# Optimization experiments

Measured on AMD Instinct MI355X. Metric: run time of the kernel, lower is better.

The kernel has to match this reference:

```python
import jax, jax.numpy as jnp
import numpy as np

N_NODES = 50000
N_EDGES = 600000
IN_CH = 128
HID = 128
OUT_CH = 1
N_GRAPHS = 64


def setup_inputs() -> dict:
    key = jax.random.key(0)
    ks = jax.random.split(key, 16)
    inp = {
        "x": jax.random.normal(ks[0], (N_NODES, IN_CH), dtype=jnp.float32),
        "edge_index": jax.random.randint(ks[1], (2, N_EDGES), 0, N_NODES, dtype=jnp.int64),
        "edge_weight": jax.random.uniform(ks[2], (N_EDGES,), dtype=jnp.float32),
        "batch": jnp.sort(jax.random.randint(ks[3], (N_NODES,), 0, N_GRAPHS, dtype=jnp.int64)),
    }
    # SAGEConv params: lin_l (neighbor-aggregate path, has bias) and lin_r (root path)
    dims = [(IN_CH, HID), (HID, HID), (HID, HID), (HID, HID)]
    for i, (din, dout) in enumerate(dims, start=1):
        s = 1.0 / np.sqrt(din)
        inp[f"Wl{i}"] = jax.random.uniform(ks[3 + 2 * i], (din, dout), minval=-s, maxval=s, dtype=jnp.float32)
        inp[f"Wr{i}"] = jax.random.uniform(ks[4 + 2 * i], (din, dout), minval=-s, maxval=s, dtype=jnp.float32)
        inp[f"b{i}"] = jnp.zeros((dout,), dtype=jnp.float32)
    s = 1.0 / np.sqrt(HID)
    inp["Wc"] = jax.random.uniform(ks[14], (HID, OUT_CH), minval=-s, maxval=s, dtype=jnp.float32)
    inp["bc"] = jnp.zeros((OUT_CH,), dtype=jnp.float32)
    return inp


def _sage_conv(x, src, dst, Wl, Wr, b):
    # mean aggregation of source-node features at each destination node
    msg = x[src]  # [E, d] gather
    agg = jax.ops.segment_sum(msg, dst, num_segments=N_NODES)
    cnt = jax.ops.segment_sum(jnp.ones((src.shape[0],), x.dtype), dst, num_segments=N_NODES)
    agg = agg / jnp.maximum(cnt, 1.0)[:, None]
    return agg @ Wl + b + x @ Wr


def reference(x, edge_index, edge_weight, batch,
              Wl1, Wr1, b1, Wl2, Wr2, b2, Wl3, Wr3, b3, Wl4, Wr4, b4, Wc, bc):
    src, dst = edge_index[0], edge_index[1]
    h = jax.nn.relu(_sage_conv(x, src, dst, Wl1, Wr1, b1))
    h = jax.nn.relu(_sage_conv(h, src, dst, Wl2, Wr2, b2))
    h = jax.nn.relu(_sage_conv(h, src, dst, Wl3, Wr3, b3))
    h = jax.nn.relu(_sage_conv(h, src, dst, Wl4, Wr4, b4))
    # global mean pool over graphs
    pooled = jax.ops.segment_sum(h, batch, num_segments=N_GRAPHS)
    gcnt = jax.ops.segment_sum(jnp.ones((N_NODES,), h.dtype), batch, num_segments=N_GRAPHS)
    pooled = pooled / jnp.maximum(gcnt, 1.0)[:, None]  # [G, HID]
    return jax.nn.sigmoid(pooled @ Wc + bc)  # [G, 1]
```

## Files before the change

kernel.cpp:

```cpp
#include <hip/hip_runtime.h>
#include <math.h>

#define NND 50000
#define LNP 50048
#define NED 600000
#define CD  128
#define NG  64
#define NBLK 196
#define GROWS 64

typedef short s8v  __attribute__((ext_vector_type(8)));
typedef float f4v  __attribute__((ext_vector_type(4)));
typedef float f2v  __attribute__((ext_vector_type(2)));
typedef unsigned short u16x4 __attribute__((ext_vector_type(4)));
typedef unsigned short u16x8 __attribute__((ext_vector_type(8)));

static __device__ __forceinline__ unsigned short f2bf(float f) {
  union { float f; unsigned u; } v; v.f = f;
  unsigned r = v.u + 0x7fffu + ((v.u >> 16) & 1u);
  return (unsigned short)(r >> 16);
}
static __device__ __forceinline__ float bf2f(unsigned short h) {
  union { unsigned u; float f; } v; v.u = ((unsigned)h) << 16; return v.f;
}
static __device__ __forceinline__ unsigned f2fp8x4(float a, float b, float c, float d) {
  int r = __builtin_amdgcn_cvt_pk_fp8_f32(a, b, 0, false);
  r = __builtin_amdgcn_cvt_pk_fp8_f32(c, d, r, true);
  return (unsigned)r;
}
static __device__ __forceinline__ void g2lds(const unsigned short* g, unsigned short* l) {
  __builtin_amdgcn_global_load_lds(
      (const __attribute__((address_space(1))) unsigned*)g,
      (__attribute__((address_space(3))) unsigned*)l, 16, 0, 0);
}

__global__ void counti_k(const int* __restrict__ idx, int* __restrict__ cnt, int n) {
  int t = blockIdx.x * blockDim.x + threadIdx.x;
  if (t < n) atomicAdd(&cnt[idx[t]], 1);
}

__global__ __launch_bounds__(256) void bsum_k(const int* __restrict__ cnt,
                                              int* __restrict__ bsum) {
  __shared__ int s[256];
  int i = blockIdx.x * 256 + threadIdx.x;
  s[threadIdx.x] = (i < NND) ? cnt[i] : 0;
  __syncthreads();
  for (int off = 128; off > 0; off >>= 1) {
    if (threadIdx.x < off) s[threadIdx.x] += s[threadIdx.x + off];
    __syncthreads();
  }
  if (threadIdx.x == 0) bsum[blockIdx.x] = s[0];
}

__global__ __launch_bounds__(256) void bscan_k(const int* __restrict__ bsum,
                                               int* __restrict__ boff,
                                               int* __restrict__ offs,
                                               const int* __restrict__ batch,
                                               int* __restrict__ gb) {
  __shared__ int s[256];
  int t = threadIdx.x;
  if (t <= NG) {
    int lo = 0, hi = NND;
    while (lo < hi) {
      int mid = (lo + hi) >> 1;
      if (batch[mid] < t) lo = mid + 1; else hi = mid;
    }
    gb[t] = lo;
  }
  s[t] = (t < NBLK) ? bsum[t] : 0;
  __syncthreads();
  for (int off = 1; off < 256; off <<= 1) {
    int v = (t >= off) ? s[t - off] : 0;
    __syncthreads();
    s[t] += v;
    __syncthreads();
  }
  if (t < NBLK) boff[t] = (t == 0) ? 0 : s[t - 1];
  if (t == NBLK - 1) offs[NND] = s[t];
}

__global__ __launch_bounds__(256) void escan_k(const int* __restrict__ cnt,
                                               const int* __restrict__ boff,
                                               int* __restrict__ offs,
                                               int* __restrict__ cur) {
  __shared__ int s[256];
  int i = blockIdx.x * 256 + threadIdx.x;
  int t = threadIdx.x;
  int v = (i < NND) ? cnt[i] : 0;
  s[t] = v;
  __syncthreads();
  for (int off = 1; off < 256; off <<= 1) {
    int u = (t >= off) ? s[t - off] : 0;
    __syncthreads();
    s[t] += u;
    __syncthreads();
  }
  if (i < NND) {
    int excl = s[t] - v + boff[blockIdx.x];
    offs[i] = excl;
    cur[i]  = excl;
  }
}

__global__ void fill_k(const int* __restrict__ src, const int* __restrict__ dst,
                       int* __restrict__ cur, int* __restrict__ csr) {
  int e = blockIdx.x * blockDim.x + threadIdx.x;
  if (e >= NED) return;
  int d = dst[e];
  int pos = atomicAdd(&cur[d], 1);
  csr[pos] = src[e];
}

struct WPtrs { const float* w[8]; unsigned short* wt[8]; };
__global__ void prep_k(const float* __restrict__ x, unsigned short* __restrict__ xb,
                       unsigned* __restrict__ x8, WPtrs p) {
  int t = blockIdx.x * blockDim.x + threadIdx.x;
  if (t < NND * 32) {
    float4 v = reinterpret_cast<const float4*>(x)[t];
    u16x4 o;
    o.x = f2bf(v.x); o.y = f2bf(v.y); o.z = f2bf(v.z); o.w = f2bf(v.w);
    reinterpret_cast<u16x4*>(xb)[t] = o;
    x8[t] = f2fp8x4(v.x, v.y, v.z, v.w);
  } else {
    int u = t - NND * 32;
    if (u < 8 * CD * CD) {
      int m = u >> 14, r = u & (CD * CD - 1);
      int n = r >> 7, k = r & 127;
      p.wt[m][r] = f2bf(p.w[m][k * CD + n]);
    }
  }
}

__global__ __launch_bounds__(256) void agg_k(const unsigned* __restrict__ xq,
                                             const int* __restrict__ csr,
                                             const int* __restrict__ offs,
                                             unsigned short* __restrict__ ab) {
  const int team = (blockIdx.x * 256 + threadIdx.x) >> 4;
  const int tl   = threadIdx.x & 15;
  const int e0 = offs[team], e1 = offs[team + 1];
  const unsigned* base = xq + tl * 2;
  f2v a01 = {0.f, 0.f}, a23 = {0.f, 0.f}, a45 = {0.f, 0.f}, a67 = {0.f, 0.f};
  int e = e0;
  for (; e + 8 <= e1; e += 8) {
    int s[8];
#pragma unroll
    for (int j = 0; j < 8; ++j) s[j] = csr[e + j];
    uint2 v[8];
#pragma unroll
    for (int j = 0; j < 8; ++j)
      v[j] = *reinterpret_cast<const uint2*>(base + (size_t)s[j] * 32);
#pragma unroll
    for (int j = 0; j < 8; ++j) {
      a01 += __builtin_amdgcn_cvt_pk_f32_fp8(v[j].x, false);
      a23 += __builtin_amdgcn_cvt_pk_f32_fp8(v[j].x, true);
      a45 += __builtin_amdgcn_cvt_pk_f32_fp8(v[j].y, false);
      a67 += __builtin_amdgcn_cvt_pk_f32_fp8(v[j].y, true);
    }
  }
  for (; e + 4 <= e1; e += 4) {
    int s[4];
#pragma unroll
    for (int j = 0; j < 4; ++j) s[j] = csr[e + j];
    uint2 v[4];
#pragma unroll
    for (int j = 0; j < 4; ++j)
      v[j] = *reinterpret_cast<const uint2*>(base + (size_t)s[j] * 32);
#pragma unroll
    for (int j = 0; j < 4; ++j) {
      a01 += __builtin_amdgcn_cvt_pk_f32_fp8(v[j].x, false);
      a23 += __builtin_amdgcn_cvt_pk_f32_fp8(v[j].x, true);
      a45 += __builtin_amdgcn_cvt_pk_f32_fp8(v[j].y, false);
      a67 += __builtin_amdgcn_cvt_pk_f32_fp8(v[j].y, true);
    }
  }
  for (; e < e1; ++e) {
    uint2 v = *reinterpret_cast<const uint2*>(base + (size_t)csr[e] * 32);
    a01 += __builtin_amdgcn_cvt_pk_f32_fp8(v.x, false);
    a23 += __builtin_amdgcn_cvt_pk_f32_fp8(v.x, true);
    a45 += __builtin_amdgcn_cvt_pk_f32_fp8(v.y, false);
    a67 += __builtin_amdgcn_cvt_pk_f32_fp8(v.y, true);
  }
  const float invd = 1.0f / fmaxf((float)(e1 - e0), 1.0f);
  u16x8 o;
  o[0] = f2bf(a01.x * invd); o[1] = f2bf(a01.y * invd);
  o[2] = f2bf(a23.x * invd); o[3] = f2bf(a23.y * invd);
  o[4] = f2bf(a45.x * invd); o[5] = f2bf(a45.y * invd);
  o[6] = f2bf(a67.x * invd); o[7] = f2bf(a67.y * invd);
  *reinterpret_cast<u16x8*>(ab + (size_t)team * CD + tl * 8) = o;
}

__global__ __launch_bounds__(256) void gemm3_k(
    const unsigned short* __restrict__ ab, const unsigned short* __restrict__ xb,
    const unsigned short* __restrict__ WlT, const unsigned short* __restrict__ WrT,
    const float* __restrict__ bias, unsigned short* __restrict__ hb,
    unsigned char* __restrict__ h8) {
  __shared__ unsigned short abuf[GROWS * CD];
  __shared__ unsigned short xbuf[GROWS * CD];

  const int tid  = threadIdx.x;
  const int wave = tid >> 6;
  const int lane = tid & 63;
  const int quad = lane >> 4;
  const int l16  = lane & 15;
  const size_t rbase = (size_t)blockIdx.x * GROWS;

#pragma unroll
  for (int j = 0; j < 4; ++j) {
    const int s = j * 256 + tid;
    const size_t goff = (rbase + (s >> 4)) * CD + (s & 15) * 8;
    g2lds(ab + goff, &abuf[(size_t)s * 8]);
    g2lds(xb + goff, &xbuf[(size_t)s * 8]);
  }

  s8v bL[2][4], bR[2][4];
#pragma unroll
  for (int nt = 0; nt < 2; ++nt) {
    const int n = wave * 32 + nt * 16 + l16;
#pragma unroll
    for (int kk = 0; kk < 4; ++kk) {
      size_t woff = (size_t)n * CD + kk * 32 + quad * 8;
      bL[nt][kk] = *reinterpret_cast<const s8v*>(WlT + woff);
      bR[nt][kk] = *reinterpret_cast<const s8v*>(WrT + woff);
    }
  }
  const float bv0 = bias[wave * 32 + l16];
  const float bv1 = bias[wave * 32 + 16 + l16];

  __syncthreads();

#pragma unroll
  for (int rt = 0; rt < GROWS / 16; ++rt) {
    const unsigned short* arow = abuf + (rt * 16 + l16) * CD + quad * 8;
    const unsigned short* xrow = xbuf + (rt * 16 + l16) * CD + quad * 8;
    f4v acc0 = {}, acc1 = {};
#pragma unroll
    for (int kk = 0; kk < 4; ++kk) {
      s8v aA = *reinterpret_cast<const s8v*>(arow + kk * 32);
      s8v aX = *reinterpret_cast<const s8v*>(xrow + kk * 32);
      acc0 = __builtin_amdgcn_mfma_f32_16x16x32_bf16(aA, bL[0][kk], acc0, 0, 0, 0);
      acc0 = __builtin_amdgcn_mfma_f32_16x16x32_bf16(aX, bR[0][kk], acc0, 0, 0, 0);
      acc1 = __builtin_amdgcn_mfma_f32_16x16x32_bf16(aA, bL[1][kk], acc1, 0, 0, 0);
      acc1 = __builtin_amdgcn_mfma_f32_16x16x32_bf16(aX, bR[1][kk], acc1, 0, 0, 0);
    }
    const size_t row0 = rbase + rt * 16 + quad * 4;
    const int c0 = wave * 32 + l16;
#pragma unroll
    for (int r = 0; r < 4; ++r) {
      const size_t row = row0 + r;
      float v0 = fmaxf(acc0[r] + bv0, 0.0f);
      float v1 = fmaxf(acc1[r] + bv1, 0.0f);
      hb[row * CD + c0]      = f2bf(v0);
      hb[row * CD + c0 + 16] = f2bf(v1);
      if (h8) {
        int p0 = __builtin_amdgcn_cvt_pk_fp8_f32(v0, v0, 0, false);
        int p1 = __builtin_amdgcn_cvt_pk_fp8_f32(v1, v1, 0, false);
        h8[row * CD + c0]      = (unsigned char)p0;
        h8[row * CD + c0 + 16] = (unsigned char)p1;
      }
    }
  }
}

__global__ __launch_bounds__(128) void pool3_k(const unsigned short* __restrict__ h,
                                               const int* __restrict__ batch,
                                               float* __restrict__ pooled) {
  const int c  = threadIdx.x;
  const int r0 = blockIdx.x * 32;
  const int rend = (r0 + 32 < NND) ? r0 + 32 : NND;
  const int g0 = batch[r0];
  const int g1 = batch[rend - 1];
  if (g0 == g1) {
    float acc = 0.f;
#pragma unroll
    for (int i = 0; i < 32; ++i) {
      int row = r0 + i;
      if (row < rend) acc += bf2f(h[(size_t)row * CD + c]);
    }
    atomicAdd(&pooled[g0 * CD + c], acc);
  } else {
    float acc = 0.f;
    int gcur = g0;
    for (int row = r0; row < rend; ++row) {
      int g = batch[row];
      if (g != gcur) {
        atomicAdd(&pooled[gcur * CD + c], acc);
        acc = 0.f; gcur = g;
      }
      acc += bf2f(h[(size_t)row * CD + c]);
    }
    atomicAdd(&pooled[gcur * CD + c], acc);
  }
}

__global__ void final_k(const float* __restrict__ pooled, const int* __restrict__ gb,
                        const float* __restrict__ Wc, const float* __restrict__ bc,
                        float* __restrict__ out) {
  int g = blockIdx.x;
  int lane = threadIdx.x;
  float part = pooled[g * CD + lane] * Wc[lane] +
               pooled[g * CD + 64 + lane] * Wc[64 + lane];
#pragma unroll
  for (int off = 32; off > 0; off >>= 1) part += __shfl_down(part, off, 64);
  if (lane == 0) {
    float cnt = (float)(gb[g + 1] - gb[g]);
    float z = part / fmaxf(cnt, 1.0f) + bc[0];
    out[g] = 1.0f / (1.0f + expf(-z));
  }
}

extern "C" void kernel_launch(void* const* d_in, const int* in_sizes, int n_in,
                              void* d_out, int out_size, void* d_ws, size_t ws_size,
                              hipStream_t stream) {
  const float* x   = (const float*)d_in[0];
  const int*   ei  = (const int*)d_in[1];
  const int*   src = ei;
  const int*   dst = ei + NED;
  const int*   batch = (const int*)d_in[3];
  const float* Wc = (const float*)d_in[16];
  const float* bc = (const float*)d_in[17];
  float* out = (float*)d_out;

  char* w = (char*)d_ws;
  auto alloc = [&](size_t bytes) {
    char* p = w; w += (bytes + 255) & ~(size_t)255; return p;
  };
  int* cnti = (int*)alloc(NND * 4);
  float* pooled = (float*)alloc(NG * CD * 4);
  size_t zspan = (size_t)(w - (char*)cnti);
  int* offs = (int*)alloc((NND + 1) * 4);
  int* cur  = (int*)alloc(NND * 4);
  int* csr  = (int*)alloc((size_t)NED * 4);
  int* gb   = (int*)alloc((NG + 1) * 4);
  int* bsum = (int*)alloc(256 * 4);
  int* boff = (int*)alloc(256 * 4);
  unsigned short* xb0 = (unsigned short*)alloc((size_t)LNP * CD * 2);
  unsigned short* xb1 = (unsigned short*)alloc((size_t)LNP * CD * 2);
  unsigned short* ab  = (unsigned short*)alloc((size_t)LNP * CD * 2);
  unsigned char* x8a = (unsigned char*)alloc((size_t)LNP * CD);
  unsigned char* x8b = (unsigned char*)alloc((size_t)LNP * CD);
  WPtrs wp;
  for (int i = 0; i < 4; ++i) {
    wp.w[2 * i]     = (const float*)d_in[4 + 3 * i];
    wp.w[2 * i + 1] = (const float*)d_in[5 + 3 * i];
  }
  for (int i = 0; i < 8; ++i) wp.wt[i] = (unsigned short*)alloc(CD * CD * 2);
  const float* bs[4] = {(const float*)d_in[6],  (const float*)d_in[9],
                        (const float*)d_in[12], (const float*)d_in[15]};

  hipMemsetAsync(cnti, 0, zspan, stream);

  counti_k<<<(NED + 255) / 256, 256, 0, stream>>>(dst, cnti, NED);
  bsum_k<<<NBLK, 256, 0, stream>>>(cnti, bsum);
  bscan_k<<<1, 256, 0, stream>>>(bsum, boff, offs, batch, gb);
  escan_k<<<NBLK, 256, 0, stream>>>(cnti, boff, offs, cur);
  fill_k<<<(NED + 255) / 256, 256, 0, stream>>>(src, dst, cur, csr);

  prep_k<<<(NND * 32 + 8 * CD * CD + 255) / 256, 256, 0, stream>>>(
      x, xb0, (unsigned*)x8a, wp);

  unsigned short* xcur = xb0;
  unsigned short* xnxt = xb1;
  unsigned char* qcur = x8a;
  unsigned char* qnxt = x8b;
  const int ggrid = LNP / GROWS;
  for (int l = 0; l < 4; ++l) {
    agg_k<<<NND * 16 / 256, 256, 0, stream>>>((const unsigned*)qcur, csr, offs, ab);
    gemm3_k<<<ggrid, 256, 0, stream>>>(ab, xcur, wp.wt[2 * l], wp.wt[2 * l + 1],
                                       bs[l], xnxt, (l < 3) ? qnxt : nullptr);
    unsigned short* t = xcur; xcur = xnxt; xnxt = t;
    unsigned char* q = qcur; qcur = qnxt; qnxt = q;
  }

  pool3_k<<<(NND + 31) / 32, 128, 0, stream>>>(xcur, batch, pooled);
  final_k<<<NG, 64, 0, stream>>>(pooled, gb, Wc, bc, out);
}
```

Measured before the change: 327.2 us.

## Fuse neighbor aggregation into SAGE GEMM kernel and fold degree count into prep

```diff
diff --git a/kernel.cpp b/kernel.cpp
--- a/kernel.cpp
+++ b/kernel.cpp
@@ -32,11 +32,6 @@
   __builtin_amdgcn_global_load_lds(
       (const __attribute__((address_space(1))) unsigned*)g,
       (__attribute__((address_space(3))) unsigned*)l, 16, 0, 0);
-}
-
-__global__ void counti_k(const int* __restrict__ idx, int* __restrict__ cnt, int n) {
-  int t = blockIdx.x * blockDim.x + threadIdx.x;
-  if (t < n) atomicAdd(&cnt[idx[t]], 1);
 }
 
 __global__ __launch_bounds__(256) void bsum_k(const int* __restrict__ cnt,
@@ -113,7 +108,8 @@
 
 struct WPtrs { const float* w[8]; unsigned short* wt[8]; };
 __global__ void prep_k(const float* __restrict__ x, unsigned short* __restrict__ xb,
-                       unsigned* __restrict__ x8, WPtrs p) {
+                       unsigned* __restrict__ x8, WPtrs p,
+                       const int* __restrict__ dst, int* __restrict__ cnt) {
   int t = blockIdx.x * blockDim.x + threadIdx.x;
   if (t < NND * 32) {
     float4 v = reinterpret_cast<const float4*>(x)[t];
@@ -127,70 +123,16 @@
       int m = u >> 14, r = u & (CD * CD - 1);
       int n = r >> 7, k = r & 127;
       p.wt[m][r] = f2bf(p.w[m][k * CD + n]);
-    }
-  }
-}
-
-__global__ __launch_bounds__(256) void agg_k(const unsigned* __restrict__ xq,
-                                             const int* __restrict__ csr,
-                                             const int* __restrict__ offs,
-                                             unsigned short* __restrict__ ab) {
-  const int team = (blockIdx.x * 256 + threadIdx.x) >> 4;
-  const int tl   = threadIdx.x & 15;
-  const int e0 = offs[team], e1 = offs[team + 1];
-  const unsigned* base = xq + tl * 2;
-  f2v a01 = {0.f, 0.f}, a23 = {0.f, 0.f}, a45 = {0.f, 0.f}, a67 = {0.f, 0.f};
-  int e = e0;
-  for (; e + 8 <= e1; e += 8) {
-    int s[8];
-#pragma unroll
-    for (int j = 0; j < 8; ++j) s[j] = csr[e + j];
-    uint2 v[8];
-#pragma unroll
-    for (int j = 0; j < 8; ++j)
-      v[j] = *reinterpret_cast<const uint2*>(base + (size_t)s[j] * 32);
-#pragma unroll
-    for (int j = 0; j < 8; ++j) {
-      a01 += __builtin_amdgcn_cvt_pk_f32_fp8(v[j].x, false);
-      a23 += __builtin_amdgcn_cvt_pk_f32_fp8(v[j].x, true);
-      a45 += __builtin_amdgcn_cvt_pk_f32_fp8(v[j].y, false);
-      a67 += __builtin_amdgcn_cvt_pk_f32_fp8(v[j].y, true);
-    }
-  }
-  for (; e + 4 <= e1; e += 4) {
-    int s[4];
-#pragma unroll
-    for (int j = 0; j < 4; ++j) s[j] = csr[e + j];
-    uint2 v[4];
-#pragma unroll
-    for (int j = 0; j < 4; ++j)
-      v[j] = *reinterpret_cast<const uint2*>(base + (size_t)s[j] * 32);
-#pragma unroll
-    for (int j = 0; j < 4; ++j) {
-      a01 += __builtin_amdgcn_cvt_pk_f32_fp8(v[j].x, false);
-      a23 += __builtin_amdgcn_cvt_pk_f32_fp8(v[j].x, true);
-      a45 += __builtin_amdgcn_cvt_pk_f32_fp8(v[j].y, false);
-      a67 += __builtin_amdgcn_cvt_pk_f32_fp8(v[j].y, true);
-    }
-  }
-  for (; e < e1; ++e) {
-    uint2 v = *reinterpret_cast<const uint2*>(base + (size_t)csr[e] * 32);
-    a01 += __builtin_amdgcn_cvt_pk_f32_fp8(v.x, false);
-    a23 += __builtin_amdgcn_cvt_pk_f32_fp8(v.x, true);
-    a45 += __builtin_amdgcn_cvt_pk_f32_fp8(v.y, false);
-    a67 += __builtin_amdgcn_cvt_pk_f32_fp8(v.y, true);
-  }
-  const float invd = 1.0f / fmaxf((float)(e1 - e0), 1.0f);
-  u16x8 o;
-  o[0] = f2bf(a01.x * invd); o[1] = f2bf(a01.y * invd);
-  o[2] = f2bf(a23.x * invd); o[3] = f2bf(a23.y * invd);
-  o[4] = f2bf(a45.x * invd); o[5] = f2bf(a45.y * invd);
-  o[6] = f2bf(a67.x * invd); o[7] = f2bf(a67.y * invd);
-  *reinterpret_cast<u16x8*>(ab + (size_t)team * CD + tl * 8) = o;
-}
-
-__global__ __launch_bounds__(256) void gemm3_k(
-    const unsigned short* __restrict__ ab, const unsigned short* __restrict__ xb,
+    } else {
+      int e = u - 8 * CD * CD;
+      if (e < NED) atomicAdd(&cnt[dst[e]], 1);
+    }
+  }
+}
+
+__global__ __launch_bounds__(256, 4) void sage_k(
+    const unsigned* __restrict__ xq, const unsigned short* __restrict__ xb,
+    const int* __restrict__ csr, const int* __restrict__ offs,
     const unsigned short* __restrict__ WlT, const unsigned short* __restrict__ WrT,
     const float* __restrict__ bias, unsigned short* __restrict__ hb,
     unsigned char* __restrict__ h8) {
@@ -207,9 +149,7 @@
 #pragma unroll
   for (int j = 0; j < 4; ++j) {
     const int s = j * 256 + tid;
-    const size_t goff = (rbase + (s >> 4)) * CD + (s & 15) * 8;
-    g2lds(ab + goff, &abuf[(size_t)s * 8]);
-    g2lds(xb + goff, &xbuf[(size_t)s * 8]);
+    g2lds(xb + (rbase + (s >> 4)) * CD + (s & 15) * 8, &xbuf[(size_t)s * 8]);
   }
 
   s8v bL[2][4], bR[2][4];
@@ -225,6 +165,65 @@
   }
   const float bv0 = bias[wave * 32 + l16];
   const float bv1 = bias[wave * 32 + 16 + l16];
+
+  const int team = tid >> 4;
+  const int tl   = tid & 15;
+  const unsigned* base = xq + tl * 2;
+  for (int i = 0; i < 4; ++i) {
+    const int rl = team * 4 + i;
+    const size_t row = rbase + rl;
+    u16x8 o = {};
+    if (row < NND) {
+      const int e0 = offs[row], e1 = offs[row + 1];
+      f2v a01 = {0.f, 0.f}, a23 = {0.f, 0.f}, a45 = {0.f, 0.f}, a67 = {0.f, 0.f};
+      int e = e0;
+      for (; e + 8 <= e1; e += 8) {
+        int s[8];
+#pragma unroll
+        for (int j = 0; j < 8; ++j) s[j] = csr[e + j];
+        uint2 v[8];
+#pragma unroll
+        for (int j = 0; j < 8; ++j)
+          v[j] = *reinterpret_cast<const uint2*>(base + (size_t)s[j] * 32);
+#pragma unroll
+        for (int j = 0; j < 8; ++j) {
+          a01 += __builtin_amdgcn_cvt_pk_f32_fp8(v[j].x, false);
+          a23 += __builtin_amdgcn_cvt_pk_f32_fp8(v[j].x, true);
+          a45 += __builtin_amdgcn_cvt_pk_f32_fp8(v[j].y, false);
+          a67 += __builtin_amdgcn_cvt_pk_f32_fp8(v[j].y, true);
+        }
+      }
+      for (; e + 4 <= e1; e += 4) {
+        int s[4];
+#pragma unroll
+        for (int j = 0; j < 4; ++j) s[j] = csr[e + j];
+        uint2 v[4];
+#pragma unroll
+        for (int j = 0; j < 4; ++j)
+          v[j] = *reinterpret_cast<const uint2*>(base + (size_t)s[j] * 32);
+#pragma unroll
+        for (int j = 0; j < 4; ++j) {
+          a01 += __builtin_amdgcn_cvt_pk_f32_fp8(v[j].x, false);
+          a23 += __builtin_amdgcn_cvt_pk_f32_fp8(v[j].x, true);
+          a45 += __builtin_amdgcn_cvt_pk_f32_fp8(v[j].y, false);
+          a67 += __builtin_amdgcn_cvt_pk_f32_fp8(v[j].y, true);
+        }
+      }
+      for (; e < e1; ++e) {
+        uint2 v = *reinterpret_cast<const uint2*>(base + (size_t)csr[e] * 32);
+        a01 += __builtin_amdgcn_cvt_pk_f32_fp8(v.x, false);
+        a23 += __builtin_amdgcn_cvt_pk_f32_fp8(v.x, true);
+        a45 += __builtin_amdgcn_cvt_pk_f32_fp8(v.y, false);
+        a67 += __builtin_amdgcn_cvt_pk_f32_fp8(v.y, true);
+      }
+      const float invd = 1.0f / fmaxf((float)(e1 - e0), 1.0f);
+      o[0] = f2bf(a01.x * invd); o[1] = f2bf(a01.y * invd);
+      o[2] = f2bf(a23.x * invd); o[3] = f2bf(a23.y * invd);
+      o[4] = f2bf(a45.x * invd); o[5] = f2bf(a45.y * invd);
+      o[6] = f2bf(a67.x * invd); o[7] = f2bf(a67.y * invd);
+    }
+    *reinterpret_cast<u16x8*>(abuf + rl * CD + tl * 8) = o;
+  }
 
   __syncthreads();
 
@@ -335,7 +334,6 @@
   int* boff = (int*)alloc(256 * 4);
   unsigned short* xb0 = (unsigned short*)alloc((size_t)LNP * CD * 2);
   unsigned short* xb1 = (unsigned short*)alloc((size_t)LNP * CD * 2);
-  unsigned short* ab  = (unsigned short*)alloc((size_t)LNP * CD * 2);
   unsigned char* x8a = (unsigned char*)alloc((size_t)LNP * CD);
   unsigned char* x8b = (unsigned char*)alloc((size_t)LNP * CD);
   WPtrs wp;
@@ -349,14 +347,13 @@
 
   hipMemsetAsync(cnti, 0, zspan, stream);
 
-  counti_k<<<(NED + 255) / 256, 256, 0, stream>>>(dst, cnti, NED);
+  prep_k<<<(NND * 32 + 8 * CD * CD + NED + 255) / 256, 256, 0, stream>>>(
+      x, xb0, (unsigned*)x8a, wp, dst, cnti);
+
   bsum_k<<<NBLK, 256, 0, stream>>>(cnti, bsum);
   bscan_k<<<1, 256, 0, stream>>>(bsum, boff, offs, batch, gb);
   escan_k<<<NBLK, 256, 0, stream>>>(cnti, boff, offs, cur);
   fill_k<<<(NED + 255) / 256, 256, 0, stream>>>(src, dst, cur, csr);
-
-  prep_k<<<(NND * 32 + 8 * CD * CD + 255) / 256, 256, 0, stream>>>(
-      x, xb0, (unsigned*)x8a, wp);
 
   unsigned short* xcur = xb0;
   unsigned short* xnxt = xb1;
@@ -364,9 +361,9 @@
   unsigned char* qnxt = x8b;
   const int ggrid = LNP / GROWS;
   for (int l = 0; l < 4; ++l) {
-    agg_k<<<NND * 16 / 256, 256, 0, stream>>>((const unsigned*)qcur, csr, offs, ab);
-    gemm3_k<<<ggrid, 256, 0, stream>>>(ab, xcur, wp.wt[2 * l], wp.wt[2 * l + 1],
-                                       bs[l], xnxt, (l < 3) ? qnxt : nullptr);
+    sage_k<<<ggrid, 256, 0, stream>>>((const unsigned*)qcur, xcur, csr, offs,
+                                      wp.wt[2 * l], wp.wt[2 * l + 1], bs[l],
+                                      xnxt, (l < 3) ? qnxt : nullptr);
     unsigned short* t = xcur; xcur = xnxt; xnxt = t;
     unsigned char* q = qcur; qcur = qnxt; qnxt = q;
   }
```

Result: no change. 327.8 us (+0.2%).
